# Performance work log

Hardware: AMD Instinct MI355X
Metric: run time of the kernel (lower is better)

## Reference

```python
import jax, jax.numpy as jnp
import numpy as np

B, N, D, H, L = 2, 1024, 256, 4, 9
HEAD = D // H  # 64
IMG_H, IMG_W = 480, 640
SINKHORN_ITERS = 20
CH = [3, 32, 64, 128, 256]


def setup_inputs() -> dict:
    key = jax.random.key(0)
    ks = iter(jax.random.split(key, 80))
    def rn(shape, s):
        return jax.random.normal(next(ks), shape, dtype=jnp.float32) * s
    inp = {}
    size = jnp.array([IMG_W, IMG_H], jnp.float32)
    inp['kpts0'] = jax.random.uniform(next(ks), (B, N, 2), dtype=jnp.float32) * size
    inp['kpts1'] = jax.random.uniform(next(ks), (B, N, 2), dtype=jnp.float32) * size
    inp['scores0'] = jax.random.uniform(next(ks), (B, N), dtype=jnp.float32)
    inp['scores1'] = jax.random.uniform(next(ks), (B, N), dtype=jnp.float32)
    inp['desc0'] = rn((B, D, N), 1.0)
    inp['desc1'] = rn((B, D, N), 1.0)
    for i in range(4):
        inp['kenc_w%d' % i] = rn((CH[i + 1], CH[i]), CH[i] ** -0.5)
        inp['kenc_b%d' % i] = rn((CH[i + 1],), 0.02)
        if i < 3:
            inp['kenc_g%d' % i] = jnp.ones((CH[i + 1],), jnp.float32)
            inp['kenc_be%d' % i] = jnp.zeros((CH[i + 1],), jnp.float32)
    s = D ** -0.5
    inp['gnn_proj_w'] = rn((L, 3, D, D), s)
    inp['gnn_proj_b'] = rn((L, 3, D), 0.02)
    inp['gnn_merge_w'] = rn((L, D, D), s)
    inp['gnn_merge_b'] = rn((L, D), 0.02)
    inp['gnn_mlp1_w'] = rn((L, 2 * D, 2 * D), (2 * D) ** -0.5)
    inp['gnn_mlp1_b'] = rn((L, 2 * D), 0.02)
    inp['gnn_ln_g'] = jnp.ones((L, 2 * D), jnp.float32)
    inp['gnn_ln_b'] = jnp.zeros((L, 2 * D), jnp.float32)
    inp['gnn_mlp2_w'] = rn((L, D, 2 * D), (2 * D) ** -0.5)
    inp['gnn_mlp2_b'] = jnp.zeros((L, D), jnp.float32)
    inp['final_w'] = rn((D, D), s)
    inp['final_b'] = rn((D,), 0.02)
    inp['bin_score'] = jnp.array(1.0, jnp.float32)
    return inp


def _conv1(x, w, b):
    # 1x1 Conv1d == per-position matmul: x [B,C,N], w [O,C], b [O]
    return jnp.einsum('oc,bcn->bon', w, x) + b[None, :, None]


def _layernorm(x, g, b, eps=1e-6):
    # matches source LayerNorm: normalize over channel dim (-2), std with ddof=1, eps added to std
    mean = jnp.mean(x, axis=1, keepdims=True)
    std = jnp.std(x, axis=1, keepdims=True, ddof=1)
    return g[None, :, None] * (x - mean) / (std + eps) + b[None, :, None]


def _normalize_kpts(kpts):
    size = jnp.array([IMG_W, IMG_H], jnp.float32)
    center = size / 2.0
    scaling = jnp.max(size) * 0.7
    return (kpts - center) / scaling


def _attn(x, src, pw, pb, mw, mb):
    # pw [3,D,D]; view(B, head_dim, n_heads, N) matches torch .view on [B,D,N]
    q = _conv1(x, pw[0], pb[0]).reshape(B, HEAD, H, -1)
    k = _conv1(src, pw[1], pb[1]).reshape(B, HEAD, H, -1)
    v = _conv1(src, pw[2], pb[2]).reshape(B, HEAD, H, -1)
    scores = jnp.einsum('bdhn,bdhm->bhnm', q, k) / (HEAD ** 0.5)
    prob = jax.nn.softmax(scores, axis=-1)
    msg = jnp.einsum('bhnm,bdhm->bdhn', prob, v).reshape(B, D, -1)
    return _conv1(msg, mw, mb)


def _sinkhorn(Z, log_mu, log_nu, iters):
    def step(uv, _):
        u, v = uv
        u = log_mu - jax.scipy.special.logsumexp(Z + v[:, None, :], axis=2)
        v = log_nu - jax.scipy.special.logsumexp(Z + u[:, :, None], axis=1)
        return (u, v), None
    init = (jnp.zeros_like(log_mu), jnp.zeros_like(log_nu))
    (u, v), _ = jax.lax.scan(step, init, None, length=iters)
    return Z + u[:, :, None] + v[:, None, :]


def _log_ot(scores, alpha, iters):
    b, m, n = scores.shape
    bins0 = jnp.broadcast_to(alpha, (b, m, 1))
    bins1 = jnp.broadcast_to(alpha, (b, 1, n))
    a = jnp.broadcast_to(alpha, (b, 1, 1))
    couplings = jnp.concatenate([jnp.concatenate([scores, bins0], -1),
                                 jnp.concatenate([bins1, a], -1)], 1)
    norm = jnp.asarray(-np.log(float(m + n)), jnp.float32)
    log_mu = jnp.concatenate([jnp.full((m,), norm, jnp.float32),
                              jnp.array([np.log(float(n))], jnp.float32) + norm])
    log_nu = jnp.concatenate([jnp.full((n,), norm, jnp.float32),
                              jnp.array([np.log(float(m))], jnp.float32) + norm])
    log_mu = jnp.broadcast_to(log_mu, (b, m + 1))
    log_nu = jnp.broadcast_to(log_nu, (b, n + 1))
    Z = _sinkhorn(couplings, log_mu, log_nu, iters)
    return Z - norm


def _superglue_fwd(kpts0, kpts1, scores0, scores1, desc0, desc1,
                   kenc_w0, kenc_b0, kenc_g0, kenc_be0,
                   kenc_w1, kenc_b1, kenc_g1, kenc_be1,
                   kenc_w2, kenc_b2, kenc_g2, kenc_be2,
                   kenc_w3, kenc_b3,
                   gnn_proj_w, gnn_proj_b, gnn_merge_w, gnn_merge_b,
                   gnn_mlp1_w, gnn_mlp1_b, gnn_ln_g, gnn_ln_b,
                   gnn_mlp2_w, gnn_mlp2_b, final_w, final_b, bin_score):
    kenc = [(kenc_w0, kenc_b0, kenc_g0, kenc_be0),
            (kenc_w1, kenc_b1, kenc_g1, kenc_be1),
            (kenc_w2, kenc_b2, kenc_g2, kenc_be2),
            (kenc_w3, kenc_b3, None, None)]

    def encode(kpts, sc):
        x = jnp.concatenate([_normalize_kpts(kpts).transpose(0, 2, 1), sc[:, None, :]], 1)  # [B,3,N]
        for (w, b, g, be) in kenc:
            x = _conv1(x, w, b)
            if g is not None:
                x = jax.nn.relu(_layernorm(x, g, be))
        return x

    desc0 = desc0 + encode(kpts0, scores0)
    desc1 = desc1 + encode(kpts1, scores1)

    # only 'cross' GNN layers execute in this fork ('self' layers are skipped via continue)
    for i in range(L):
        def prop(x, src):
            msg = _attn(x, src, gnn_proj_w[i], gnn_proj_b[i], gnn_merge_w[i], gnn_merge_b[i])
            y = jnp.concatenate([x, msg], 1)  # [B,2D,N]
            y = jax.nn.relu(_layernorm(_conv1(y, gnn_mlp1_w[i], gnn_mlp1_b[i]), gnn_ln_g[i], gnn_ln_b[i]))
            return _conv1(y, gnn_mlp2_w[i], gnn_mlp2_b[i])
        d0 = prop(desc0, desc1)
        d1 = prop(desc1, desc0)
        desc0, desc1 = desc0 + d0, desc1 + d1

    mdesc0 = _conv1(desc0, final_w, final_b)
    mdesc1 = _conv1(desc1, final_w, final_b)
    sc = jnp.einsum('bdn,bdm->bnm', mdesc0, mdesc1) / (D ** 0.5)
    return _log_ot(sc, bin_score, SINKHORN_ITERS)  # [B, N+1, N+1] log assignment matrix


def reference(kpts0, kpts1, scores0, scores1, desc0, desc1,
              kenc_w0, kenc_b0, kenc_g0, kenc_be0,
              kenc_w1, kenc_b1, kenc_g1, kenc_be1,
              kenc_w2, kenc_b2, kenc_g2, kenc_be2,
              kenc_w3, kenc_b3,
              gnn_proj_w, gnn_proj_b, gnn_merge_w, gnn_merge_b,
              gnn_mlp1_w, gnn_mlp1_b, gnn_ln_g, gnn_ln_b,
              gnn_mlp2_w, gnn_mlp2_b, final_w, final_b, bin_score):
    return _superglue_fwd(kpts0, kpts1, scores0, scores1, desc0, desc1,
                          kenc_w0, kenc_b0, kenc_g0, kenc_be0,
                          kenc_w1, kenc_b1, kenc_g1, kenc_be1,
                          kenc_w2, kenc_b2, kenc_g2, kenc_be2,
                          kenc_w3, kenc_b3,
                          gnn_proj_w, gnn_proj_b, gnn_merge_w, gnn_merge_b,
                          gnn_mlp1_w, gnn_mlp1_b, gnn_ln_g, gnn_ln_b,
                          gnn_mlp2_w, gnn_mlp2_b, final_w, final_b, bin_score)
```

## Files before the change

### kernel.cpp

```cpp
#include <hip/hip_runtime.h>
#include <hip/hip_bf16.h>
#include <math.h>

#define DEVI static __device__ __forceinline__

namespace {
constexpr int Bc   = 2;
constexpr int Nc   = 1024;
constexpr int Dc   = 256;
constexpr int NP1c = 1025;
constexpr int LDZ  = 1028;
constexpr int LDV  = 1028;
constexpr float LN_EPS = 1e-6f;
constexpr float NORMV  = -7.6246189861593985f;
constexpr float LOGNV  =  6.9314718055994531f;
}

typedef __attribute__((ext_vector_type(8))) short bf16x8;
typedef __attribute__((ext_vector_type(4))) float f32x4;

DEVI void split2(float v, __hip_bfloat16& h, __hip_bfloat16& l) {
    h = __float2bfloat16(v);
    l = __float2bfloat16(v - __bfloat162float(h));
}

DEVI float bf2f(short u) { return __uint_as_float(((unsigned)(unsigned short)u) << 16); }

#define GLDS16(gp, lp) __builtin_amdgcn_global_load_lds( \
    (const __attribute__((address_space(1))) void*)(gp), \
    (__attribute__((address_space(3))) void*)(lp), 16, 0, 0)

DEVI float block_sum_256(float v, float* scratch) {
    int t = threadIdx.x;
    scratch[t] = v;
    __syncthreads();
    for (int s = 128; s > 0; s >>= 1) {
        if (t < s) scratch[t] += scratch[t + s];
        __syncthreads();
    }
    float r = scratch[0];
    __syncthreads();
    return r;
}

DEVI void ln_relu_inplace(float* x, const float* g, const float* be, int C, float* scratch) {
    int t = threadIdx.x;
    float v = (t < C) ? x[t] : 0.f;
    float mean = block_sum_256(v, scratch) / (float)C;
    float dv = (t < C) ? (x[t] - mean) : 0.f;
    float var = block_sum_256(dv * dv, scratch) / (float)(C - 1);
    float rstd = 1.f / (sqrtf(var) + LN_EPS);
    if (t < C) x[t] = fmaxf(g[t] * dv * rstd + be[t], 0.f);
    __syncthreads();
}

__global__ void transpose_desc(const float* __restrict__ d0, const float* __restrict__ d1,
                               float* __restrict__ dst)
{
    __shared__ float tile[32][33];
    const int db = blockIdx.z, dir = db >> 1, b = db & 1;
    const float* src = dir ? d1 : d0;
    const int n0 = blockIdx.x * 32, c0 = blockIdx.y * 32;
    const int tx = threadIdx.x, ty = threadIdx.y;
    for (int cc = ty; cc < 32; cc += 8)
        tile[cc][tx] = src[((long)b * 256 + c0 + cc) * 1024 + n0 + tx];
    __syncthreads();
    for (int nn = ty; nn < 32; nn += 8)
        dst[((long)db * 1024 + n0 + nn) * 256 + c0 + tx] = tile[tx][nn];
}

__global__ __launch_bounds__(256) void kenc_kernel(
    const float* __restrict__ kpts0, const float* __restrict__ kpts1,
    const float* __restrict__ scr0, const float* __restrict__ scr1,
    const float* __restrict__ descT,
    float* __restrict__ descF,
    __hip_bfloat16* __restrict__ catHi, __hip_bfloat16* __restrict__ catLo,
    const float* __restrict__ w0, const float* __restrict__ b0,
    const float* __restrict__ g0, const float* __restrict__ be0,
    const float* __restrict__ w1T, const float* __restrict__ b1,
    const float* __restrict__ g1, const float* __restrict__ be1,
    const float* __restrict__ w2T, const float* __restrict__ b2,
    const float* __restrict__ g2, const float* __restrict__ be2,
    const float* __restrict__ w3T, const float* __restrict__ b3)
{
    __shared__ float xa[256], xb[256], scratch[256];
    const int n = blockIdx.x, db = blockIdx.y, t = threadIdx.x;
    const int dir = db >> 1, b = db & 1;
    const float* kpts = dir ? kpts1 : kpts0;
    const float* scr  = dir ? scr1  : scr0;
    if (t == 0) {
        float kx = kpts[((long)b * Nc + n) * 2 + 0];
        float ky = kpts[((long)b * Nc + n) * 2 + 1];
        xa[0] = (kx - 320.f) * (1.f / 448.f);
        xa[1] = (ky - 240.f) * (1.f / 448.f);
        xa[2] = scr[b * Nc + n];
    }
    __syncthreads();
    if (t < 32) { float a = b0[t]; for (int c = 0; c < 3;  ++c) a += w0[t*3 + c] * xa[c]; xb[t] = a; }
    __syncthreads();
    ln_relu_inplace(xb, g0, be0, 32, scratch);
    if (t < 64) {
        float a = b1[t];
        #pragma unroll 8
        for (int c = 0; c < 32;  ++c) a += w1T[c*64 + t] * xb[c];
        xa[t] = a;
    }
    __syncthreads();
    ln_relu_inplace(xa, g1, be1, 64, scratch);
    if (t < 128) {
        float a = b2[t];
        #pragma unroll 8
        for (int c = 0; c < 64;  ++c) a += w2T[c*128 + t] * xa[c];
        xb[t] = a;
    }
    __syncthreads();
    ln_relu_inplace(xb, g2, be2, 128, scratch);
    {   float a = b3[t];
        #pragma unroll 8
        for (int c = 0; c < 128; ++c) a += w3T[c*256 + t] * xb[c];
        float v = descT[((long)db * Nc + n) * Dc + t] + a;
        descF[((long)db * Nc + n) * Dc + t] = v;
        __hip_bfloat16 h, l; split2(v, h, l);
        long cr = ((long)db * Nc + n) * 512 + t;
        catHi[cr] = h; catLo[cr] = l;
    }
}

__global__ __launch_bounds__(256) void transposeW(
    const float* __restrict__ src, float* __restrict__ dst, int O, int C)
{
    long i = (long)blockIdx.x * 256 + threadIdx.x;
    if (i >= (long)O * C) return;
    int o = (int)(i / C), c = (int)(i % C);
    dst[(long)c * O + o] = src[i];
}

template<int BM, int BN, int EPI, int BLO, int ALO, int BKC>
__global__ __launch_bounds__(256) void mfma_nt(
    const short* __restrict__ Ahi0, const short* __restrict__ Alo0, int lda,
    const short* __restrict__ Bhi0, const short* __restrict__ Blo0, int ldb,
    int K, float scale, const float* __restrict__ bias,
    float* __restrict__ outF, __hip_bfloat16* __restrict__ outHi,
    __hip_bfloat16* __restrict__ outLo,
    __hip_bfloat16* __restrict__ outHi2, __hip_bfloat16* __restrict__ outHi3,
    int ldo,
    long aS1, long bS1, long oS1)
{
    constexpr int MI = BM / 32;
    constexpr int NI = BN / 32;
    constexpr int instA = BM / 16, instB = BN / 16;
    constexpr int OFF_AH = 0;
    constexpr int OFF_AL = BM * 32;
    constexpr int OFF_BH = (1 + ALO) * BM * 32;
    constexpr int OFF_BL = OFF_BH + BN * 32;
    constexpr int CHUNK = ((1 + ALO) * BM + (1 + BLO) * BN) * 32;
    __shared__ short smem[BKC * CHUNK];

    const int z = blockIdx.z;
    const long aOff = z * aS1, bOff = z * bS1, oOff = z * oS1;
    const short* Ah = Ahi0 + aOff;
    const short* Al = ALO ? (Alo0 + aOff) : nullptr;
    const short* Bh = Bhi0 + bOff;
    const short* Bl = BLO ? (Blo0 + bOff) : nullptr;

    const int m0 = blockIdx.y * BM, n0 = blockIdx.x * BN;
    const int t = threadIdx.x, lane = t & 63, wid = t >> 6;
    const int lr = lane & 15, lg = lane >> 4;
    const int wr = wid >> 1, wc = wid & 1;

    f32x4 acc[MI][NI];
    for (int mi = 0; mi < MI; ++mi)
        for (int ni = 0; ni < NI; ++ni)
            acc[mi][ni] = f32x4{0.f, 0.f, 0.f, 0.f};

    for (int k0 = 0; k0 < K; k0 += 32 * BKC) {
        constexpr int total = (1 + ALO) * instA + (1 + BLO) * instB;
        for (int q = wid; q < total; q += 4) {
            const short* gsrc; int ldg, mi, ploff, row0;
            if (q < instA)                      { gsrc = Ah; ldg = lda; mi = q;          ploff = OFF_AH; row0 = m0; }
            else if (ALO && q < 2 * instA)      { gsrc = Al; ldg = lda; mi = q - instA;  ploff = OFF_AL; row0 = m0; }
            else {
                int rb = q - (1 + ALO) * instA;
                if (rb < instB) { gsrc = Bh; mi = rb;         ploff = OFF_BH; }
                else            { gsrc = Bl; mi = rb - instB; ploff = OFF_BL; }
                ldg = ldb; row0 = n0;
            }
            const short* g = gsrc + (long)(row0 + mi * 16 + lr) * ldg + (k0 + lg * 8);
            #pragma unroll
            for (int c = 0; c < BKC; ++c)
                GLDS16(g + 32 * c, smem + c * CHUNK + ploff + mi * 512);
        }
        __syncthreads();
        #pragma unroll
        for (int kc2 = 0; kc2 < BKC; ++kc2) {
            const short* sm2 = smem + kc2 * CHUNK;
            bf16x8 ah[MI], al[MI];
            #pragma unroll
            for (int mi = 0; mi < MI; ++mi) {
                ah[mi] = *(const bf16x8*)(sm2 + OFF_AH + ((wr * MI + mi) * 64 + lane) * 8);
                if (ALO) al[mi] = *(const bf16x8*)(sm2 + OFF_AL + ((wr * MI + mi) * 64 + lane) * 8);
            }
            #pragma unroll
            for (int ni = 0; ni < NI; ++ni) {
                bf16x8 bh = *(const bf16x8*)(sm2 + OFF_BH + ((wc * NI + ni) * 64 + lane) * 8);
                #pragma unroll
                for (int mi = 0; mi < MI; ++mi) {
                    acc[mi][ni] = __builtin_amdgcn_mfma_f32_16x16x32_bf16(ah[mi], bh, acc[mi][ni], 0, 0, 0);
                    if (ALO) acc[mi][ni] = __builtin_amdgcn_mfma_f32_16x16x32_bf16(al[mi], bh, acc[mi][ni], 0, 0, 0);
                }
                if (BLO) {
                    bf16x8 bl = *(const bf16x8*)(sm2 + OFF_BL + ((wc * NI + ni) * 64 + lane) * 8);
                    #pragma unroll
                    for (int mi = 0; mi < MI; ++mi)
                        acc[mi][ni] = __builtin_amdgcn_mfma_f32_16x16x32_bf16(ah[mi], bl, acc[mi][ni], 0, 0, 0);
                }
            }
        }
        __syncthreads();
    }

    for (int mi = 0; mi < MI; ++mi) {
        for (int i = 0; i < 4; ++i) {
            int row = m0 + wr * (BM / 2) + mi * 16 + lg * 4 + i;
            for (int ni = 0; ni < NI; ++ni) {
                int col = n0 + wc * (BN / 2) + ni * 16 + lr;
                float v = acc[mi][ni][i] * scale;
                if (bias) v += bias[col];
                if (EPI == 0) {
                    outF[(long)row * ldo + col + oOff] = v;
                } else if (EPI == 1) {
                    __hip_bfloat16 h, l;
                    split2(v, h, l);
                    outHi[(long)row * ldo + col + oOff] = h;
                    outLo[(long)row * ldo + col + oOff] = l;
                } else if (EPI == 2) {
                    int dirb = row >> 10, rloc = row & 1023;
                    int tq = col >> 8, within = col & 255;
                    int h4 = within >> 6, hd = within & 63;
                    __hip_bfloat16 hh = __float2bfloat16(v);
                    if (tq == 2) {
                        int w2 = rloc >> 8, mloc = rloc & 255;
                        int lane2 = ((mloc & 31) >> 3) * 16 + (hd & 15);
                        long idx = ((((long)(dirb*4+h4)*4 + w2)*8 + (mloc>>5))*4 + (hd>>4))*512 + lane2*8 + (mloc&7);
                        outHi2[idx] = hh;
                    } else {
                        int lane2 = ((hd & 31) >> 3) * 16 + (rloc & 15);
                        long idx = (((long)(dirb*4+h4)*64 + (rloc>>4))*2 + (hd>>5))*512 + lane2*8 + (hd&7);
                        if (tq == 0) outHi[idx] = hh;
                        else         outHi3[idx] = hh;
                    }
                } else if (EPI == 3) {
                    long i256 = (long)row * 256 + col;
                    v += outF[i256];
                    outF[i256] = v;
                    __hip_bfloat16 h, l;
                    split2(v, h, l);
                    outHi[(long)row * 512 + col] = h;
                    outLo[(long)row * 512 + col] = l;
                } else {
                    outHi[(long)row * ldo + col + oOff] = __float2bfloat16(v);
                }
            }
        }
    }
}

__global__ __launch_bounds__(256) void attn_fused(
    const __hip_bfloat16* __restrict__ qFh,
    const __hip_bfloat16* __restrict__ kFh, const __hip_bfloat16* __restrict__ vFh,
    __hip_bfloat16* __restrict__ catHi)
{
    __shared__ short pLds[4 * 16 * 256];
    __shared__ float redm[4][16], reds[4][16];
    const int y = blockIdx.y;
    const int dir = y >> 3, b = (y >> 2) & 1, h = y & 3;
    const int q0 = blockIdx.x * 16;
    const int t = threadIdx.x, lane = t & 63, w = t >> 6;
    const int lr = lane & 15, lg = lane >> 4;
    const int dbQ = dir * 2 + b;
    const int srcdb = (1 - dir) * 2 + b;
    const short* qh = (const short*)qFh;
    const short* kh = (const short*)kFh;
    const short* vh = (const short*)vFh;

    const long qbase = (((long)(dbQ * 4 + h)) * 64 + (q0 >> 4)) * 2;
    bf16x8 ah[2];
    #pragma unroll
    for (int kc = 0; kc < 2; ++kc)
        ah[kc] = *(const bf16x8*)(qh + (qbase + kc) * 512 + lane * 8);

    f32x4 acc[16];
    #pragma unroll
    for (int ni = 0; ni < 16; ++ni) acc[ni] = f32x4{0.f, 0.f, 0.f, 0.f};

    const long kbase0 = (((long)(srcdb * 4 + h)) * 64 + w * 16) * 2;
    #pragma unroll
    for (int ni = 0; ni < 16; ++ni) {
        long kb = (kbase0 + ni * 2) * 512 + lane * 8;
        bf16x8 bh0 = *(const bf16x8*)(kh + kb);
        bf16x8 bh1 = *(const bf16x8*)(kh + kb + 512);
        acc[ni] = __builtin_amdgcn_mfma_f32_16x16x32_bf16(ah[0], bh0, acc[ni], 0, 0, 0);
        acc[ni] = __builtin_amdgcn_mfma_f32_16x16x32_bf16(ah[1], bh1, acc[ni], 0, 0, 0);
    }

    float mx[4] = {-1e30f, -1e30f, -1e30f, -1e30f};
    #pragma unroll
    for (int ni = 0; ni < 16; ++ni)
        #pragma unroll
        for (int i = 0; i < 4; ++i) {
            float v = acc[ni][i] * 0.125f;
            acc[ni][i] = v;
            mx[i] = fmaxf(mx[i], v);
        }
    #pragma unroll
    for (int off = 1; off < 16; off <<= 1)
        #pragma unroll
        for (int i = 0; i < 4; ++i) mx[i] = fmaxf(mx[i], __shfl_xor(mx[i], off));
    if (lr == 0)
        #pragma unroll
        for (int i = 0; i < 4; ++i) redm[w][lg * 4 + i] = mx[i];
    __syncthreads();
    float Mv[4];
    #pragma unroll
    for (int i = 0; i < 4; ++i)
        Mv[i] = fmaxf(fmaxf(redm[0][lg*4+i], redm[1][lg*4+i]),
                      fmaxf(redm[2][lg*4+i], redm[3][lg*4+i]));
    float sm[4] = {0.f, 0.f, 0.f, 0.f};
    #pragma unroll
    for (int ni = 0; ni < 16; ++ni)
        #pragma unroll
        for (int i = 0; i < 4; ++i) {
            float e = __expf(acc[ni][i] - Mv[i]);
            acc[ni][i] = e;
            sm[i] += e;
        }
    #pragma unroll
    for (int off = 1; off < 16; off <<= 1)
        #pragma unroll
        for (int i = 0; i < 4; ++i) sm[i] += __shfl_xor(sm[i], off);
    if (lr == 0)
        #pragma unroll
        for (int i = 0; i < 4; ++i) reds[w][lg * 4 + i] = sm[i];
    __syncthreads();
    float inv[4];
    #pragma unroll
    for (int i = 0; i < 4; ++i)
        inv[i] = 1.f / (reds[0][lg*4+i] + reds[1][lg*4+i] + reds[2][lg*4+i] + reds[3][lg*4+i]);

    char* pB = (char*)pLds + w * 8192;
    #pragma unroll
    for (int ni = 0; ni < 16; ++ni)
        #pragma unroll
        for (int i = 0; i < 4; ++i) {
            int q = lg * 4 + i, m = ni * 16 + lr;
            int byte = (q * 512 + m * 2) ^ ((q & 7) << 4);
            *(short*)(pB + byte) = (short)__bfloat16_as_ushort(__float2bfloat16(acc[ni][i] * inv[i]));
        }
    __syncthreads();

    f32x4 acc2[4];
    #pragma unroll
    for (int bi = 0; bi < 4; ++bi) acc2[bi] = f32x4{0.f, 0.f, 0.f, 0.f};
    const long vbase0 = (((long)(srcdb * 4 + h)) * 4 + w) * 8;
    #pragma unroll
    for (int km = 0; km < 8; ++km) {
        int rb = (lr * 512 + km * 64 + lg * 16) ^ ((lr & 7) << 4);
        bf16x8 pa = *(const bf16x8*)(pB + rb);
        #pragma unroll
        for (int bi = 0; bi < 4; ++bi) {
            long vr = ((vbase0 + km) * 4 + bi) * 512 + lane * 8;
            bf16x8 vhf = *(const bf16x8*)(vh + vr);
            acc2[bi] = __builtin_amdgcn_mfma_f32_16x16x32_bf16(pa, vhf, acc2[bi], 0, 0, 0);
        }
    }
    __syncthreads();
    float* pr = (float*)pLds;
    #pragma unroll
    for (int bi = 0; bi < 4; ++bi)
        #pragma unroll
        for (int i = 0; i < 4; ++i)
            pr[w * 1024 + (lg * 4 + i) * 64 + bi * 16 + lr] = acc2[bi][i];
    __syncthreads();
    #pragma unroll
    for (int k = 0; k < 4; ++k) {
        int e = t + k * 256;
        float v = pr[e] + pr[1024 + e] + pr[2048 + e] + pr[3072 + e];
        int q = e >> 6, d = e & 63;
        long a = ((long)dbQ * 1024 + q0 + q) * 512 + 256 + h * 64 + d;
        catHi[a] = __float2bfloat16(v);
    }
}

__global__ __launch_bounds__(256) void ln_relu_w(
    __hip_bfloat16* __restrict__ y, const float* __restrict__ g, const float* __restrict__ be)
{
    const int t = threadIdx.x, lane = t & 63, w = t >> 6;
    const long row = (long)blockIdx.x * 4 + w;
    short* src = (short*)y + row * 512;
    bf16x8 r = *(const bf16x8*)(src + lane * 8);
    float xv[8];
    #pragma unroll
    for (int k = 0; k < 8; ++k) xv[k] = bf2f(r[k]);
    float s = 0.f, q = 0.f;
    #pragma unroll
    for (int k = 0; k < 8; ++k) { s += xv[k]; q += xv[k] * xv[k]; }
    #pragma unroll
    for (int off = 1; off < 64; off <<= 1) {
        s += __shfl_xor(s, off);
        q += __shfl_xor(q, off);
    }
    float mean = s / 512.f;
    float var = fmaxf((q - 512.f * mean * mean) / 511.f, 0.f);
    float rstd = 1.f / (sqrtf(var) + LN_EPS);
    float4 g0 = ((const float4*)g)[lane * 2], g1 = ((const float4*)g)[lane * 2 + 1];
    float4 b0 = ((const float4*)be)[lane * 2], b1 = ((const float4*)be)[lane * 2 + 1];
    float gv[8] = {g0.x, g0.y, g0.z, g0.w, g1.x, g1.y, g1.z, g1.w};
    float bv[8] = {b0.x, b0.y, b0.z, b0.w, b1.x, b1.y, b1.z, b1.w};
    bf16x8 outv;
    #pragma unroll
    for (int k = 0; k < 8; ++k) {
        float o = fmaxf(gv[k] * (xv[k] - mean) * rstd + bv[k], 0.f);
        outv[k] = (short)__bfloat16_as_ushort(__float2bfloat16(o));
    }
    *(bf16x8*)(src + lane * 8) = outv;
}

__global__ __launch_bounds__(256) void wconv_hi(
    const float* __restrict__ w, __hip_bfloat16* __restrict__ hi, long total)
{
    long i = (long)blockIdx.x * 256 + threadIdx.x;
    if (i >= total) return;
    hi[i] = __float2bfloat16(w[i]);
}

__global__ __launch_bounds__(256) void wconv_proj(
    const float* __restrict__ w, __hip_bfloat16* __restrict__ hi)
{
    long i = (long)blockIdx.x * 256 + threadIdx.x;
    if (i >= 9L * 768 * 256) return;
    long l9 = i / (768 * 256);
    int rem = (int)(i % (768 * 256));
    int op = rem / 256, c = rem % 256;
    int tq = op / 256, within = op % 256;
    int h = within / 64, hd = within % 64;
    int o = tq * 256 + hd * 4 + h;
    hi[i] = __float2bfloat16(w[(l9 * 768 + o) * 256 + c]);
}

__global__ void wconv_proj_bias(const float* __restrict__ b, float* __restrict__ bp)
{
    int i = blockIdx.x * 256 + threadIdx.x;
    if (i >= 9 * 768) return;
    int l9 = i / 768, op = i % 768;
    int tq = op / 256, within = op % 256;
    int h = within / 64, hd = within % 64;
    bp[i] = b[(l9 * 3 + tq) * 256 + hd * 4 + h];
}

__global__ __launch_bounds__(256) void wconv_mergeT(
    const float* __restrict__ w, __hip_bfloat16* __restrict__ hi, __hip_bfloat16* __restrict__ lo)
{
    long i = (long)blockIdx.x * 256 + threadIdx.x;
    if (i >= 9L * 256 * 256) return;
    long l9 = i / (256 * 256);
    int rem = (int)(i % (256 * 256));
    int c = rem / 256, j = rem % 256;
    int h = c / 64, hd = c % 64;
    float v = w[(l9 * 256 + j) * 256 + (hd * 4 + h)];
    __hip_bfloat16 hh, ll; split2(v, hh, ll);
    hi[i] = hh; lo[i] = ll;
}

__global__ __launch_bounds__(256) void wconv_m1(
    const float* __restrict__ w,
    __hip_bfloat16* __restrict__ m1cHi,
    __hip_bfloat16* __restrict__ m1bHi, __hip_bfloat16* __restrict__ m1bLo)
{
    long i = (long)blockIdx.x * 256 + threadIdx.x;
    if (i >= 9L * 512 * 512) return;
    long lo9 = i / 512;
    int c = (int)(i % 512);
    if (c < 256) {
        m1cHi[lo9 * 512 + c] = __float2bfloat16(w[i]);
    } else {
        __hip_bfloat16 hh, ll; split2(w[i], hh, ll);
        m1bHi[lo9 * 256 + c - 256] = hh; m1bLo[lo9 * 256 + c - 256] = ll;
    }
}

__global__ __launch_bounds__(64) void bias_fold(
    const float* __restrict__ w1, const float* __restrict__ b1,
    const float* __restrict__ bm, float* __restrict__ out)
{
    int og = blockIdx.x;
    int l = og >> 9, o = og & 511;
    int t = threadIdx.x;
    float s = 0.f;
    for (int j = t; j < 256; j += 64)
        s += w1[((long)l * 512 + o) * 512 + 256 + j] * bm[l * 256 + j];
    for (int off = 32; off > 0; off >>= 1) s += __shfl_down(s, off);
    if (t == 0) out[og] = b1[(long)l * 512 + o] + s;
}

__global__ void bins_fill(float* __restrict__ Z, const float* __restrict__ alpha_p)
{
    float alpha = alpha_p[0];
    int idx = blockIdx.x * 256 + threadIdx.x;
    int b = blockIdx.y;
    float* Zb = Z + (long)b * NP1c * LDZ;
    if (idx < NP1c) Zb[(long)1024 * LDZ + idx] = alpha;
    else { int i = idx - NP1c; if (i < 1024) Zb[(long)i * LDZ + 1024] = alpha; }
}

__global__ void transpose_np1(const float* __restrict__ Z, float* __restrict__ ZT)
{
    __shared__ float tile[32][33];
    int b = blockIdx.z;
    int i0 = blockIdx.y * 32, j0 = blockIdx.x * 32;
    int tx = threadIdx.x, ty = threadIdx.y;
    const float* Zb = Z + (long)b * NP1c * LDZ;
    float* Tb = ZT + (long)b * NP1c * LDZ;
    for (int ii = ty; ii < 32; ii += 8) {
        int i = i0 + ii, j = j0 + tx;
        if (i < NP1c && j < NP1c) tile[ii][tx] = Zb[(long)i * LDZ + j];
    }
    __syncthreads();
    for (int jj = ty; jj < 32; jj += 8) {
        int j = j0 + jj, i = i0 + tx;
        if (j < NP1c && i < NP1c) Tb[(long)j * LDZ + i] = tile[tx][jj];
    }
}

__global__ void zero_vec2(float* __restrict__ a, float* __restrict__ b, int n)
{
    int i = blockIdx.x * 256 + threadIdx.x;
    if (i < n) { a[i] = 0.f; b[i] = 0.f; }
}

__global__ __launch_bounds__(256) void sinkhorn_lse(
    const float* __restrict__ M, const float* __restrict__ addv, float* __restrict__ outv)
{
    const int t = threadIdx.x, lane = t & 63, w = t >> 6;
    long rowid = (long)blockIdx.x * 4 + w;
    if (rowid >= 2 * NP1c) return;
    int b = rowid >= NP1c ? 1 : 0;
    int i = (int)(rowid - (long)b * NP1c);
    const float* row = M + ((long)b * NP1c + i) * LDZ;
    const float* av = addv + (long)b * LDV;
    float m = -1e30f, s = 0.f;
    #pragma unroll
    for (int k = 0; k < 4; ++k) {
        float4 x = ((const float4*)row)[lane * 4 + k];
        float4 a = ((const float4*)av)[lane * 4 + k];
        float u0 = x.x + a.x, u1 = x.y + a.y, u2 = x.z + a.z, u3 = x.w + a.w;
        float mk = fmaxf(fmaxf(u0, u1), fmaxf(u2, u3));
        float sk = __expf(u0 - mk) + __expf(u1 - mk) + __expf(u2 - mk) + __expf(u3 - mk);
        if (mk > m) { s = s * __expf(m - mk) + sk; m = mk; }
        else        { s += sk * __expf(mk - m); }
    }
    if (lane == 0) {
        float v4 = row[1024] + av[1024];
        if (v4 > m) { s = s * __expf(m - v4) + 1.f; m = v4; }
        else        { s += __expf(v4 - m); }
    }
    #pragma unroll
    for (int off = 1; off < 64; off <<= 1) {
        float m2 = __shfl_xor(m, off);
        float s2 = __shfl_xor(s, off);
        float mm = fmaxf(m, m2);
        s = s * __expf(m - mm) + s2 * __expf(m2 - mm);
        m = mm;
    }
    if (lane == 0) {
        float lse = m + __logf(s);
        float lmu = (i < 1024) ? NORMV : (LOGNV + NORMV);
        outv[(long)b * LDV + i] = lmu - lse;
    }
}

__global__ __launch_bounds__(256) void final_out_k(
    const float* __restrict__ Z, const float* __restrict__ u,
    const float* __restrict__ v, float* __restrict__ outp)
{
    const int i = blockIdx.x, b = blockIdx.y, t = threadIdx.x;
    const float* row = Z + ((long)b * NP1c + i) * LDZ;
    float* orow = outp + ((long)b * NP1c + i) * NP1c;
    float ui = u[(long)b * LDV + i];
    for (int j = t; j < NP1c; j += 256)
        orow[j] = row[j] + ui + v[(long)b * LDV + j] - NORMV;
}

extern "C" void kernel_launch(void* const* d_in, const int* in_sizes, int n_in,
                              void* d_out, int out_size, void* d_ws, size_t ws_size,
                              hipStream_t stream)
{
    (void)in_sizes; (void)n_in; (void)out_size; (void)ws_size;
    const float* kpts0   = (const float*)d_in[0];
    const float* kpts1   = (const float*)d_in[1];
    const float* scores0 = (const float*)d_in[2];
    const float* scores1 = (const float*)d_in[3];
    const float* desc0   = (const float*)d_in[4];
    const float* desc1   = (const float*)d_in[5];
    const float* kw0 = (const float*)d_in[6];  const float* kb0 = (const float*)d_in[7];
    const float* kg0 = (const float*)d_in[8];  const float* ke0 = (const float*)d_in[9];
    const float* kw1 = (const float*)d_in[10]; const float* kb1 = (const float*)d_in[11];
    const float* kg1 = (const float*)d_in[12]; const float* ke1 = (const float*)d_in[13];
    const float* kw2 = (const float*)d_in[14]; const float* kb2 = (const float*)d_in[15];
    const float* kg2 = (const float*)d_in[16]; const float* ke2 = (const float*)d_in[17];
    const float* kw3 = (const float*)d_in[18]; const float* kb3 = (const float*)d_in[19];
    const float* gnn_proj_w  = (const float*)d_in[20];
    const float* gnn_proj_b  = (const float*)d_in[21];
    const float* gnn_merge_w = (const float*)d_in[22];
    const float* gnn_merge_b = (const float*)d_in[23];
    const float* gnn_mlp1_w  = (const float*)d_in[24];
    const float* gnn_mlp1_b  = (const float*)d_in[25];
    const float* gnn_ln_g    = (const float*)d_in[26];
    const float* gnn_ln_b    = (const float*)d_in[27];
    const float* gnn_mlp2_w  = (const float*)d_in[28];
    const float* gnn_mlp2_b  = (const float*)d_in[29];
    const float* final_w     = (const float*)d_in[30];
    const float* final_b     = (const float*)d_in[31];
    const float* bin_score   = (const float*)d_in[32];

    char* wsb = (char*)d_ws;
    size_t off = 0;
    auto alloc = [&](size_t bytes) -> void* {
        void* p = wsb + off;
        off = (off + bytes + 255) & ~(size_t)255;
        return p;
    };
    typedef __hip_bfloat16 bf;
    const long ROWS = 4L * Nc;
    float* descF  = (float*)alloc(ROWS * 256 * 4);
    float* descT  = (float*)alloc(ROWS * 256 * 4);
    float* Zm     = (float*)alloc((long)Bc * NP1c * LDZ * 4);
    float* ZT     = (float*)alloc((long)Bc * NP1c * LDZ * 4);
    float* uvec   = (float*)alloc(Bc * LDV * 4);
    float* vvec   = (float*)alloc(Bc * LDV * 4);
    float* projBp = (float*)alloc(9L * 768 * 4);
    float* b1c    = (float*)alloc(9L * 512 * 4);
    float* kw1T   = (float*)alloc(32L * 64 * 4);
    float* kw2T   = (float*)alloc(64L * 128 * 4);
    float* kw3T   = (float*)alloc(128L * 256 * 4);
    bf* catHi = (bf*)alloc(ROWS * 512 * 2);  bf* catLo = (bf*)alloc(ROWS * 512 * 2);
    bf* qFh = (bf*)alloc(1048576 * 2);
    bf* kFh = (bf*)alloc(1048576 * 2);
    bf* vFh = (bf*)alloc(1048576 * 2);
    bf* ybHi  = (bf*)alloc(ROWS * 512 * 2);
    bf* mdHi  = (bf*)alloc(ROWS * 256 * 2);  bf* mdLo  = (bf*)alloc(ROWS * 256 * 2);
    bf* projHi = (bf*)alloc(9L*768*256*2);
    bf* mrgTHi = (bf*)alloc(9L*256*256*2);   bf* mrgTLo = (bf*)alloc(9L*256*256*2);
    bf* m1bHi  = (bf*)alloc(9L*512*256*2);   bf* m1bLo  = (bf*)alloc(9L*512*256*2);
    bf* m1cHi  = (bf*)alloc(9L*512*512*2);
    bf* m2Hi   = (bf*)alloc(9L*256*512*2);
    bf* finHi  = (bf*)alloc(256L*256*2);

    wconv_proj<<<dim3((9*768*256+255)/256), 256, 0, stream>>>(gnn_proj_w, projHi);
    wconv_proj_bias<<<dim3(27), 256, 0, stream>>>(gnn_proj_b, projBp);
    wconv_mergeT<<<dim3((9*256*256+255)/256), 256, 0, stream>>>(gnn_merge_w, mrgTHi, mrgTLo);
    wconv_m1<<<dim3((int)((9L*512*512+255)/256)), 256, 0, stream>>>(gnn_mlp1_w, m1cHi, m1bHi, m1bLo);
    wconv_hi<<<dim3((9*256*512+255)/256), 256, 0, stream>>>(gnn_mlp2_w, m2Hi, 9L*256*512);
    wconv_hi<<<dim3((256*256+255)/256), 256, 0, stream>>>(final_w, finHi, 256L*256);
    bias_fold<<<dim3(9*512), 64, 0, stream>>>(gnn_mlp1_w, gnn_mlp1_b, gnn_merge_b, b1c);
    transposeW<<<dim3((64*32+255)/256), 256, 0, stream>>>(kw1, kw1T, 64, 32);
    transposeW<<<dim3((128*64+255)/256), 256, 0, stream>>>(kw2, kw2T, 128, 64);
    transposeW<<<dim3((256*128+255)/256), 256, 0, stream>>>(kw3, kw3T, 256, 128);
    mfma_nt<128,128,4,1,1,2><<<dim3(2,4,9), 256, 0, stream>>>(
        (const short*)m1bHi, (const short*)m1bLo, 256,
        (const short*)mrgTHi, (const short*)mrgTLo, 256,
        256, 1.f, nullptr,
        nullptr, m1cHi + 256, nullptr, nullptr, nullptr, 512,
        512L*256, 256L*256, 512L*512);

    transpose_desc<<<dim3(32,8,4), dim3(32,8), 0, stream>>>(desc0, desc1, descT);
    kenc_kernel<<<dim3(Nc, 4), 256, 0, stream>>>(
        kpts0, kpts1, scores0, scores1, descT, descF, catHi, catLo,
        kw0, kb0, kg0, ke0, kw1T, kb1, kg1, ke1, kw2T, kb2, kg2, ke2, kw3T, kb3);

    for (int l = 0; l < 9; ++l) {
        mfma_nt<64,64,2,0,0,4><<<dim3(12,64,1), 256, 0, stream>>>(
            (const short*)catHi, nullptr, 512,
            (const short*)(projHi + (long)l*768*256), nullptr, 256,
            256, 1.f, projBp + (long)l*768,
            nullptr, qFh, nullptr, vFh, kFh, 0,
            0, 0, 0);
        attn_fused<<<dim3(64, 16), 256, 0, stream>>>(qFh, kFh, vFh, catHi);
        mfma_nt<64,64,4,0,0,4><<<dim3(8,64,1), 256, 0, stream>>>(
            (const short*)catHi, nullptr, 512,
            (const short*)(m1cHi + (long)l*512*512), nullptr, 512,
            512, 1.f, b1c + (long)l*512,
            nullptr, ybHi, nullptr, nullptr, nullptr, 512,
            0, 0, 0);
        ln_relu_w<<<dim3(1024), 256, 0, stream>>>(
            ybHi, gnn_ln_g + (long)l*512, gnn_ln_b + (long)l*512);
        mfma_nt<64,64,3,0,0,4><<<dim3(4,64,1), 256, 0, stream>>>(
            (const short*)ybHi, nullptr, 512,
            (const short*)(m2Hi + (long)l*256*512), nullptr, 512,
            512, 1.f, gnn_mlp2_b + (long)l*256,
            descF, catHi, catLo, nullptr, nullptr, 0,
            0, 0, 0);
    }

    mfma_nt<64,64,1,0,1,4><<<dim3(4,64,1), 256, 0, stream>>>(
        (const short*)catHi, (const short*)catLo, 512,
        (const short*)finHi, nullptr, 256,
        256, 1.f, final_b,
        nullptr, mdHi, mdLo, nullptr, nullptr, 256,
        0, 0, 0);
    mfma_nt<64,64,0,1,1,4><<<dim3(16,16,2), 256, 0, stream>>>(
        (const short*)mdHi, (const short*)mdLo, 256,
        (const short*)mdHi + 2048L*256, (const short*)mdLo + 2048L*256, 256,
        256, 1.f/16.f, nullptr,
        Zm, nullptr, nullptr, nullptr, nullptr, LDZ,
        1024L*256, 1024L*256, (long)NP1c*LDZ);
    bins_fill<<<dim3(9,2), 256, 0, stream>>>(Zm, bin_score);

    transpose_np1<<<dim3(33,33,2), dim3(32,8), 0, stream>>>(Zm, ZT);
    zero_vec2<<<dim3((2*LDV+255)/256), 256, 0, stream>>>(uvec, vvec, Bc * LDV);
    for (int it = 0; it < 20; ++it) {
        sinkhorn_lse<<<dim3(513), 256, 0, stream>>>(Zm, vvec, uvec);
        sinkhorn_lse<<<dim3(513), 256, 0, stream>>>(ZT, uvec, vvec);
    }
    final_out_k<<<dim3(NP1c, Bc), 256, 0, stream>>>(Zm, uvec, vvec, (float*)d_out);
}
```

Baseline: 881.9 us.

## Run Sinkhorn on bf16 score copies and double attention query tile

The Sinkhorn log-sum-exp iterations now read bf16 copies of the score matrix and its transpose, produced in the transpose kernel, which halves the bytes streamed on each of the 40 passes. The final output still uses the fp32 scores. Separately, attn_fused now processes 32 queries per block instead of 16, so each loaded K/V fragment feeds twice as many MFMAs and the grid is halved. Rounding the scores to bf16 inside Sinkhorn loses precision in the dual potentials, and the larger attention tile raises register and LDS use.

After: 898.1 us. About the same (+1.8%).

```diff
diff --git a/kernel.cpp b/kernel.cpp
--- a/kernel.cpp
+++ b/kernel.cpp
@@ -10,6 +10,7 @@
 constexpr int Dc   = 256;
 constexpr int NP1c = 1025;
 constexpr int LDZ  = 1028;
+constexpr int LDZB = 1032;
 constexpr int LDV  = 1028;
 constexpr float LN_EPS = 1e-6f;
 constexpr float NORMV  = -7.6246189861593985f;
@@ -270,11 +271,11 @@
     const __hip_bfloat16* __restrict__ kFh, const __hip_bfloat16* __restrict__ vFh,
     __hip_bfloat16* __restrict__ catHi)
 {
-    __shared__ short pLds[4 * 16 * 256];
-    __shared__ float redm[4][16], reds[4][16];
+    __shared__ short pLds[4 * 32 * 256];
+    __shared__ float redm[4][32], reds[4][32];
     const int y = blockIdx.y;
     const int dir = y >> 3, b = (y >> 2) & 1, h = y & 3;
-    const int q0 = blockIdx.x * 16;
+    const int q0 = blockIdx.x * 32;
     const int t = threadIdx.x, lane = t & 63, w = t >> 6;
     const int lr = lane & 15, lg = lane >> 4;
     const int dbQ = dir * 2 + b;
@@ -283,15 +284,20 @@
     const short* kh = (const short*)kFh;
     const short* vh = (const short*)vFh;
 
-    const long qbase = (((long)(dbQ * 4 + h)) * 64 + (q0 >> 4)) * 2;
-    bf16x8 ah[2];
-    #pragma unroll
-    for (int kc = 0; kc < 2; ++kc)
-        ah[kc] = *(const bf16x8*)(qh + (qbase + kc) * 512 + lane * 8);
-
-    f32x4 acc[16];
-    #pragma unroll
-    for (int ni = 0; ni < 16; ++ni) acc[ni] = f32x4{0.f, 0.f, 0.f, 0.f};
+    bf16x8 ah[2][2];
+    #pragma unroll
+    for (int r = 0; r < 2; ++r)
+        #pragma unroll
+        for (int kc = 0; kc < 2; ++kc) {
+            long qb = (((long)(dbQ * 4 + h)) * 64 + (q0 >> 4) + r) * 2 + kc;
+            ah[r][kc] = *(const bf16x8*)(qh + qb * 512 + lane * 8);
+        }
+
+    f32x4 acc[2][16];
+    #pragma unroll
+    for (int r = 0; r < 2; ++r)
+        #pragma unroll
+        for (int ni = 0; ni < 16; ++ni) acc[r][ni] = f32x4{0.f, 0.f, 0.f, 0.f};
 
     const long kbase0 = (((long)(srcdb * 4 + h)) * 64 + w * 16) * 2;
     #pragma unroll
@@ -299,94 +305,132 @@
         long kb = (kbase0 + ni * 2) * 512 + lane * 8;
         bf16x8 bh0 = *(const bf16x8*)(kh + kb);
         bf16x8 bh1 = *(const bf16x8*)(kh + kb + 512);
-        acc[ni] = __builtin_amdgcn_mfma_f32_16x16x32_bf16(ah[0], bh0, acc[ni], 0, 0, 0);
-        acc[ni] = __builtin_amdgcn_mfma_f32_16x16x32_bf16(ah[1], bh1, acc[ni], 0, 0, 0);
-    }
-
-    float mx[4] = {-1e30f, -1e30f, -1e30f, -1e30f};
-    #pragma unroll
-    for (int ni = 0; ni < 16; ++ni)
+        #pragma unroll
+        for (int r = 0; r < 2; ++r) {
+            acc[r][ni] = __builtin_amdgcn_mfma_f32_16x16x32_bf16(ah[r][0], bh0, acc[r][ni], 0, 0, 0);
+            acc[r][ni] = __builtin_amdgcn_mfma_f32_16x16x32_bf16(ah[r][1], bh1, acc[r][ni], 0, 0, 0);
+        }
+    }
+
+    float mx[2][4];
+    #pragma unroll
+    for (int r = 0; r < 2; ++r)
+        #pragma unroll
+        for (int i = 0; i < 4; ++i) mx[r][i] = -1e30f;
+    #pragma unroll
+    for (int r = 0; r < 2; ++r)
+        #pragma unroll
+        for (int ni = 0; ni < 16; ++ni)
+            #pragma unroll
+            for (int i = 0; i < 4; ++i) {
+                float v = acc[r][ni][i] * 0.125f;
+                acc[r][ni][i] = v;
+                mx[r][i] = fmaxf(mx[r][i], v);
+            }
+    #pragma unroll
+    for (int off = 1; off < 16; off <<= 1)
+        #pragma unroll
+        for (int r = 0; r < 2; ++r)
+            #pragma unroll
+            for (int i = 0; i < 4; ++i) mx[r][i] = fmaxf(mx[r][i], __shfl_xor(mx[r][i], off));
+    if (lr == 0)
+        #pragma unroll
+        for (int r = 0; r < 2; ++r)
+            #pragma unroll
+            for (int i = 0; i < 4; ++i) redm[w][r * 16 + lg * 4 + i] = mx[r][i];
+    __syncthreads();
+    float Mv[2][4];
+    #pragma unroll
+    for (int r = 0; r < 2; ++r)
         #pragma unroll
         for (int i = 0; i < 4; ++i) {
-            float v = acc[ni][i] * 0.125f;
-            acc[ni][i] = v;
-            mx[i] = fmaxf(mx[i], v);
-        }
+            int qq = r * 16 + lg * 4 + i;
+            Mv[r][i] = fmaxf(fmaxf(redm[0][qq], redm[1][qq]), fmaxf(redm[2][qq], redm[3][qq]));
+        }
+    float sm[2][4] = {};
+    #pragma unroll
+    for (int r = 0; r < 2; ++r)
+        #pragma unroll
+        for (int ni = 0; ni < 16; ++ni)
+            #pragma unroll
+            for (int i = 0; i < 4; ++i) {
+                float e = __expf(acc[r][ni][i] - Mv[r][i]);
+                acc[r][ni][i] = e;
+                sm[r][i] += e;
+            }
     #pragma unroll
     for (int off = 1; off < 16; off <<= 1)
         #pragma unroll
-        for (int i = 0; i < 4; ++i) mx[i] = fmaxf(mx[i], __shfl_xor(mx[i], off));
+        for (int r = 0; r < 2; ++r)
+            #pragma unroll
+            for (int i = 0; i < 4; ++i) sm[r][i] += __shfl_xor(sm[r][i], off);
     if (lr == 0)
         #pragma unroll
-        for (int i = 0; i < 4; ++i) redm[w][lg * 4 + i] = mx[i];
-    __syncthreads();
-    float Mv[4];
-    #pragma unroll
-    for (int i = 0; i < 4; ++i)
-        Mv[i] = fmaxf(fmaxf(redm[0][lg*4+i], redm[1][lg*4+i]),
-                      fmaxf(redm[2][lg*4+i], redm[3][lg*4+i]));
-    float sm[4] = {0.f, 0.f, 0.f, 0.f};
-    #pragma unroll
-    for (int ni = 0; ni < 16; ++ni)
+        for (int r = 0; r < 2; ++r)
+            #pragma unroll
+            for (int i = 0; i < 4; ++i) reds[w][r * 16 + lg * 4 + i] = sm[r][i];
+    __syncthreads();
+    float inv[2][4];
+    #pragma unroll
+    for (int r = 0; r < 2; ++r)
         #pragma unroll
         for (int i = 0; i < 4; ++i) {
-            float e = __expf(acc[ni][i] - Mv[i]);
-            acc[ni][i] = e;
-            sm[i] += e;
-        }
-    #pragma unroll
-    for (int off = 1; off < 16; off <<= 1)
-        #pragma unroll
-        for (int i = 0; i < 4; ++i) sm[i] += __shfl_xor(sm[i], off);
-    if (lr == 0)
-        #pragma unroll
-        for (int i = 0; i < 4; ++i) reds[w][lg * 4 + i] = sm[i];
-    __syncthreads();
-    float inv[4];
-    #pragma unroll
-    for (int i = 0; i < 4; ++i)
-        inv[i] = 1.f / (reds[0][lg*4+i] + reds[1][lg*4+i] + reds[2][lg*4+i] + reds[3][lg*4+i]);
-
-    char* pB = (char*)pLds + w * 8192;
-    #pragma unroll
-    for (int ni = 0; ni < 16; ++ni)
-        #pragma unroll
-        for (int i = 0; i < 4; ++i) {
-            int q = lg * 4 + i, m = ni * 16 + lr;
-            int byte = (q * 512 + m * 2) ^ ((q & 7) << 4);
-            *(short*)(pB + byte) = (short)__bfloat16_as_ushort(__float2bfloat16(acc[ni][i] * inv[i]));
-        }
-    __syncthreads();
-
-    f32x4 acc2[4];
-    #pragma unroll
-    for (int bi = 0; bi < 4; ++bi) acc2[bi] = f32x4{0.f, 0.f, 0.f, 0.f};
+            int qq = r * 16 + lg * 4 + i;
+            inv[r][i] = 1.f / (reds[0][qq] + reds[1][qq] + reds[2][qq] + reds[3][qq]);
+        }
+
+    char* pB = (char*)pLds + w * 16384;
+    #pragma unroll
+    for (int r = 0; r < 2; ++r)
+        #pragma unroll
+        for (int ni = 0; ni < 16; ++ni)
+            #pragma unroll
+            for (int i = 0; i < 4; ++i) {
+                int qq = r * 16 + lg * 4 + i, m = ni * 16 + lr;
+                int byte = (qq * 512 + m * 2) ^ ((qq & 7) << 4);
+                *(short*)(pB + byte) = (short)__bfloat16_as_ushort(__float2bfloat16(acc[r][ni][i] * inv[r][i]));
+            }
+    __syncthreads();
+
+    f32x4 acc2[2][4];
+    #pragma unroll
+    for (int r = 0; r < 2; ++r)
+        #pragma unroll
+        for (int bi = 0; bi < 4; ++bi) acc2[r][bi] = f32x4{0.f, 0.f, 0.f, 0.f};
     const long vbase0 = (((long)(srcdb * 4 + h)) * 4 + w) * 8;
     #pragma unroll
     for (int km = 0; km < 8; ++km) {
-        int rb = (lr * 512 + km * 64 + lg * 16) ^ ((lr & 7) << 4);
-        bf16x8 pa = *(const bf16x8*)(pB + rb);
+        bf16x8 pa[2];
+        #pragma unroll
+        for (int r = 0; r < 2; ++r) {
+            int rb = ((r * 16 + lr) * 512 + km * 64 + lg * 16) ^ ((lr & 7) << 4);
+            pa[r] = *(const bf16x8*)(pB + rb);
+        }
         #pragma unroll
         for (int bi = 0; bi < 4; ++bi) {
             long vr = ((vbase0 + km) * 4 + bi) * 512 + lane * 8;
             bf16x8 vhf = *(const bf16x8*)(vh + vr);
-            acc2[bi] = __builtin_amdgcn_mfma_f32_16x16x32_bf16(pa, vhf, acc2[bi], 0, 0, 0);
+            #pragma unroll
+            for (int r = 0; r < 2; ++r)
+                acc2[r][bi] = __builtin_amdgcn_mfma_f32_16x16x32_bf16(pa[r], vhf, acc2[r][bi], 0, 0, 0);
         }
     }
     __syncthreads();
     float* pr = (float*)pLds;
     #pragma unroll
-    for (int bi = 0; bi < 4; ++bi)
-        #pragma unroll
-        for (int i = 0; i < 4; ++i)
-            pr[w * 1024 + (lg * 4 + i) * 64 + bi * 16 + lr] = acc2[bi][i];
-    __syncthreads();
-    #pragma unroll
-    for (int k = 0; k < 4; ++k) {
+    for (int r = 0; r < 2; ++r)
+        #pragma unroll
+        for (int bi = 0; bi < 4; ++bi)
+            #pragma unroll
+            for (int i = 0; i < 4; ++i)
+                pr[w * 2048 + (r * 16 + lg * 4 + i) * 64 + bi * 16 + lr] = acc2[r][bi][i];
+    __syncthreads();
+    #pragma unroll
+    for (int k = 0; k < 8; ++k) {
         int e = t + k * 256;
-        float v = pr[e] + pr[1024 + e] + pr[2048 + e] + pr[3072 + e];
-        int q = e >> 6, d = e & 63;
-        long a = ((long)dbQ * 1024 + q0 + q) * 512 + 256 + h * 64 + d;
+        float v = pr[e] + pr[2048 + e] + pr[4096 + e] + pr[6144 + e];
+        int qq = e >> 6, d = e & 63;
+        long a = ((long)dbQ * 1024 + q0 + qq) * 512 + 256 + h * 64 + d;
         catHi[a] = __float2bfloat16(v);
     }
 }
@@ -512,22 +556,28 @@
     else { int i = idx - NP1c; if (i < 1024) Zb[(long)i * LDZ + 1024] = alpha; }
 }
 
-__global__ void transpose_np1(const float* __restrict__ Z, float* __restrict__ ZT)
+__global__ void transpose_convert(const float* __restrict__ Z,
+                                  __hip_bfloat16* __restrict__ Zb,
+                                  __hip_bfloat16* __restrict__ ZTb)
 {
     __shared__ float tile[32][33];
     int b = blockIdx.z;
     int i0 = blockIdx.y * 32, j0 = blockIdx.x * 32;
     int tx = threadIdx.x, ty = threadIdx.y;
-    const float* Zb = Z + (long)b * NP1c * LDZ;
-    float* Tb = ZT + (long)b * NP1c * LDZ;
+    const float* Zs = Z + (long)b * NP1c * LDZ;
     for (int ii = ty; ii < 32; ii += 8) {
         int i = i0 + ii, j = j0 + tx;
-        if (i < NP1c && j < NP1c) tile[ii][tx] = Zb[(long)i * LDZ + j];
+        if (i < NP1c && j < NP1c) {
+            float v = Zs[(long)i * LDZ + j];
+            tile[ii][tx] = v;
+            Zb[((long)b * NP1c + i) * LDZB + j] = __float2bfloat16(v);
+        }
     }
     __syncthreads();
     for (int jj = ty; jj < 32; jj += 8) {
         int j = j0 + jj, i = i0 + tx;
-        if (j < NP1c && i < NP1c) Tb[(long)j * LDZ + i] = tile[tx][jj];
+        if (j < NP1c && i < NP1c)
+            ZTb[((long)b * NP1c + j) * LDZB + i] = __float2bfloat16(tile[tx][jj]);
     }
 }
 
@@ -537,29 +587,36 @@
     if (i < n) { a[i] = 0.f; b[i] = 0.f; }
 }
 
-__global__ __launch_bounds__(256) void sinkhorn_lse(
-    const float* __restrict__ M, const float* __restrict__ addv, float* __restrict__ outv)
+__global__ __launch_bounds__(256) void sinkhorn_lse_bf(
+    const __hip_bfloat16* __restrict__ M, const float* __restrict__ addv, float* __restrict__ outv)
 {
     const int t = threadIdx.x, lane = t & 63, w = t >> 6;
     long rowid = (long)blockIdx.x * 4 + w;
     if (rowid >= 2 * NP1c) return;
     int b = rowid >= NP1c ? 1 : 0;
     int i = (int)(rowid - (long)b * NP1c);
-    const float* row = M + ((long)b * NP1c + i) * LDZ;
+    const short* row = (const short*)M + ((long)b * NP1c + i) * LDZB;
     const float* av = addv + (long)b * LDV;
-    float m = -1e30f, s = 0.f;
+    bf16x8 x0 = *(const bf16x8*)(row + lane * 16);
+    bf16x8 x1 = *(const bf16x8*)(row + lane * 16 + 8);
+    float u[16];
     #pragma unroll
     for (int k = 0; k < 4; ++k) {
-        float4 x = ((const float4*)row)[lane * 4 + k];
         float4 a = ((const float4*)av)[lane * 4 + k];
-        float u0 = x.x + a.x, u1 = x.y + a.y, u2 = x.z + a.z, u3 = x.w + a.w;
-        float mk = fmaxf(fmaxf(u0, u1), fmaxf(u2, u3));
-        float sk = __expf(u0 - mk) + __expf(u1 - mk) + __expf(u2 - mk) + __expf(u3 - mk);
-        if (mk > m) { s = s * __expf(m - mk) + sk; m = mk; }
-        else        { s += sk * __expf(mk - m); }
-    }
+        int e = k * 4;
+        u[e+0] = ((e+0 < 8) ? bf2f(x0[e+0]) : bf2f(x1[e-8+0])) + a.x;
+        u[e+1] = ((e+1 < 8) ? bf2f(x0[e+1]) : bf2f(x1[e-8+1])) + a.y;
+        u[e+2] = ((e+2 < 8) ? bf2f(x0[e+2]) : bf2f(x1[e-8+2])) + a.z;
+        u[e+3] = ((e+3 < 8) ? bf2f(x0[e+3]) : bf2f(x1[e-8+3])) + a.w;
+    }
+    float m = -1e30f;
+    #pragma unroll
+    for (int k = 0; k < 16; ++k) m = fmaxf(m, u[k]);
+    float s = 0.f;
+    #pragma unroll
+    for (int k = 0; k < 16; ++k) s += __expf(u[k] - m);
     if (lane == 0) {
-        float v4 = row[1024] + av[1024];
+        float v4 = bf2f(row[1024]) + av[1024];
         if (v4 > m) { s = s * __expf(m - v4) + 1.f; m = v4; }
         else        { s += __expf(v4 - m); }
     }
@@ -634,7 +691,6 @@
     float* descF  = (float*)alloc(ROWS * 256 * 4);
     float* descT  = (float*)alloc(ROWS * 256 * 4);
     float* Zm     = (float*)alloc((long)Bc * NP1c * LDZ * 4);
-    float* ZT     = (float*)alloc((long)Bc * NP1c * LDZ * 4);
     float* uvec   = (float*)alloc(Bc * LDV * 4);
     float* vvec   = (float*)alloc(Bc * LDV * 4);
     float* projBp = (float*)alloc(9L * 768 * 4);
@@ -642,6 +698,8 @@
     float* kw1T   = (float*)alloc(32L * 64 * 4);
     float* kw2T   = (float*)alloc(64L * 128 * 4);
     float* kw3T   = (float*)alloc(128L * 256 * 4);
+    bf* Zb  = (bf*)alloc((long)Bc * NP1c * LDZB * 2);
+    bf* ZTb = (bf*)alloc((long)Bc * NP1c * LDZB * 2);
     bf* catHi = (bf*)alloc(ROWS * 512 * 2);  bf* catLo = (bf*)alloc(ROWS * 512 * 2);
     bf* qFh = (bf*)alloc(1048576 * 2);
     bf* kFh = (bf*)alloc(1048576 * 2);
@@ -684,7 +742,7 @@
             256, 1.f, projBp + (long)l*768,
             nullptr, qFh, nullptr, vFh, kFh, 0,
             0, 0, 0);
-        attn_fused<<<dim3(64, 16), 256, 0, stream>>>(qFh, kFh, vFh, catHi);
+        attn_fused<<<dim3(32, 16), 256, 0, stream>>>(qFh, kFh, vFh, catHi);
         mfma_nt<64,64,4,0,0,4><<<dim3(8,64,1), 256, 0, stream>>>(
             (const short*)catHi, nullptr, 512,
             (const short*)(m1cHi + (long)l*512*512), nullptr, 512,
@@ -715,11 +773,11 @@
         1024L*256, 1024L*256, (long)NP1c*LDZ);
     bins_fill<<<dim3(9,2), 256, 0, stream>>>(Zm, bin_score);
 
-    transpose_np1<<<dim3(33,33,2), dim3(32,8), 0, stream>>>(Zm, ZT);
+    transpose_convert<<<dim3(33,33,2), dim3(32,8), 0, stream>>>(Zm, Zb, ZTb);
     zero_vec2<<<dim3((2*LDV+255)/256), 256, 0, stream>>>(uvec, vvec, Bc * LDV);
     for (int it = 0; it < 20; ++it) {
-        sinkhorn_lse<<<dim3(513), 256, 0, stream>>>(Zm, vvec, uvec);
-        sinkhorn_lse<<<dim3(513), 256, 0, stream>>>(ZT, uvec, vvec);
+        sinkhorn_lse_bf<<<dim3(513), 256, 0, stream>>>(Zb,  vvec, uvec);
+        sinkhorn_lse_bf<<<dim3(513), 256, 0, stream>>>(ZTb, uvec, vvec);
     }
     final_out_k<<<dim3(NP1c, Bc), 256, 0, stream>>>(Zm, uvec, vvec, (float*)d_out);
 }
```
